# Kernel tuning notes

Measured on AMD Instinct MI355X. Metric: run time of the kernel, lower is better.

The kernel has to match this reference:

```python
import jax, jax.numpy as jnp
import numpy as np

N = 128   # n_features == out_dim (required by the Christoffel permutes)
H = 256   # MLP hidden width of forward_func
B = 16    # batch size (state_batch is [2B, N])
EPS_G = 1e-4
EPS_DG = 1e-6
EPS_V = 1e-6


def setup_inputs() -> dict:
    key = jax.random.key(0)
    ks = jax.random.split(key, 6)
    return {
        "t": jax.random.uniform(ks[0], (), dtype=jnp.float32),
        "state_batch": jax.random.normal(ks[1], (2 * B, N), dtype=jnp.float32) * 0.1,
        "x0_batch": jax.random.normal(ks[2], (B, N), dtype=jnp.float32),
        "x1_batch": jax.random.normal(ks[3], (B, N), dtype=jnp.float32),
        "W1": jax.random.normal(ks[4], (N, H), dtype=jnp.float32) / np.float32(np.sqrt(N)),
        "b1": jnp.zeros((H,), dtype=jnp.float32),
        "W2": jax.random.normal(ks[5], (H, N), dtype=jnp.float32) / np.float32(np.sqrt(H)),
        "b2": jnp.zeros((N,), dtype=jnp.float32),
    }


def reference(t, state_batch, x0_batch, x1_batch, W1, b1, W2, b2):
    def f(x):  # forward_func, per-sample: [N] -> [N]
        return jnp.tanh(x @ W1 + b1) @ W2 + b2

    def metric(x):  # G(x) = J J^T + 1e-4 I, per-sample: [N] -> [N, N]
        J = jax.jacrev(f)(x)                      # [N, N], matches per-output grad loop
        return J @ J.T + EPS_G * jnp.eye(N, dtype=x.dtype)

    deviation, dev_velocity = jnp.split(state_batch, 2, axis=0)  # each [B, N]
    window = 4.0 * t * (1.0 - t)
    # x along the perturbed straight path
    x = x0_batch + t * (x1_batch - x0_batch) + window * deviation  # [B, N]

    # dG[b, i, j, k] = dG_ij/dx_k -- replaces the out_dim^2 autograd.grad loop
    dG = jax.vmap(jax.jacfwd(metric))(x)  # [B, N, N, N]
    nrm = jnp.sqrt(jnp.sum(dG * dG, axis=(1, 2, 3), keepdims=True))
    dG = dG / (nrm + EPS_DG)

    # Christoffel-like symbols
    Gamma = 0.5 * (dG + jnp.transpose(dG, (0, 2, 1, 3)) - jnp.transpose(dG, (0, 3, 1, 2)))
    a = -jnp.einsum('bijk,bj,bk->bi', Gamma, dev_velocity, dev_velocity)
    a = a / (jnp.linalg.norm(dev_velocity, axis=1, keepdims=True) + EPS_V)

    restoration = -0.1 * deviation
    return jnp.concatenate([dev_velocity, a + restoration], axis=0)  # [2B, N]
```

## Files before the change

### kernel.cpp

```cpp
#include <hip/hip_runtime.h>
#include <math.h>


static constexpr int OFF_W2T  = 0;
static constexpr int OFF_S    = 32768;
static constexpr int OFF_Q    = 98304;
static constexpr int OFF_D    = 163840;
static constexpr int OFF_C    = 167936;
static constexpr int OFF_UV   = 172032;
static constexpr int OFF_AV   = 176128;
static constexpr int OFF_VN   = 180224;
static constexpr int OFF_SUM  = 180240;
static constexpr int OFF_PT   = 180256;
static constexpr int OFF_PN   = OFF_PT + 16 * 32768;

__global__ __launch_bounds__(256) void k_stage1(const float* __restrict__ tptr,
                                                const float* __restrict__ state,
                                                const float* __restrict__ x0,
                                                const float* __restrict__ x1,
                                                const float* __restrict__ W1,
                                                const float* __restrict__ b1,
                                                const float* __restrict__ W2,
                                                float* __restrict__ ws,
                                                float* __restrict__ out) {
    __shared__ __align__(16) float smem[2 * 32 * 34];
    int blk = blockIdx.x;
    int tid = threadIdx.x;

    if (blk < 64) {
        float* Ai = smem;
        float* Aj = smem + 1088;
        int m0 = (blk >> 3) * 32, n0 = (blk & 7) * 32;
        int lx = tid & 31, lr = tid >> 5;
        int tx = tid & 15, ty = tid >> 4;
        float a00 = 0, a01 = 0, a10 = 0, a11 = 0;
        for (int kc = 0; kc < 128; kc += 32) {
            #pragma unroll
            for (int i = 0; i < 4; ++i) {
                int k = lr + 8 * i;
                Ai[k * 34 + lx] = W1[(kc + k) * 256 + m0 + lx];
                Aj[k * 34 + lx] = W1[(kc + k) * 256 + n0 + lx];
            }
            __syncthreads();
            #pragma unroll
            for (int k = 0; k < 32; ++k) {
                float2 a = *(const float2*)&Ai[k * 34 + 2 * ty];
                float2 b = *(const float2*)&Aj[k * 34 + 2 * tx];
                a00 += a.x * b.x; a01 += a.x * b.y;
                a10 += a.y * b.x; a11 += a.y * b.y;
            }
            __syncthreads();
        }
        float* S = ws + OFF_S;
        int m = m0 + 2 * ty, n = n0 + 2 * tx;
        S[m * 256 + n]           = a00;
        S[m * 256 + n + 1]       = a01;
        S[(m + 1) * 256 + n]     = a10;
        S[(m + 1) * 256 + n + 1] = a11;
    } else if (blk < 128) {
        float* Xi = smem;
        float* Xj = smem + 1088;
        int bq = blk - 64;
        int m0 = (bq >> 3) * 32, n0 = (bq & 7) * 32;
        int lx = tid & 31, lr = tid >> 5;
        int tx = tid & 15, ty = tid >> 4;
        float a00 = 0, a01 = 0, a10 = 0, a11 = 0;
        for (int kc = 0; kc < 128; kc += 32) {
            #pragma unroll
            for (int i = 0; i < 4; ++i) {
                Xi[lx * 34 + lr + 8 * i] = W2[(m0 + lr + 8 * i) * 128 + kc + lx];
                Xj[lx * 34 + lr + 8 * i] = W2[(n0 + lr + 8 * i) * 128 + kc + lx];
            }
            __syncthreads();
            #pragma unroll
            for (int k = 0; k < 32; ++k) {
                float2 a = *(const float2*)&Xi[k * 34 + 2 * ty];
                float2 b = *(const float2*)&Xj[k * 34 + 2 * tx];
                a00 += a.x * b.x; a01 += a.x * b.y;
                a10 += a.y * b.x; a11 += a.y * b.y;
            }
            __syncthreads();
        }
        float* Q = ws + OFF_Q;
        int m = m0 + 2 * ty, n = n0 + 2 * tx;
        Q[m * 256 + n]           = a00;
        Q[m * 256 + n + 1]       = a01;
        Q[(m + 1) * 256 + n]     = a10;
        Q[(m + 1) * 256 + n + 1] = a11;
    } else if (blk < 160) {
        float* tile = smem;
        int b2 = blk - 128;
        int c0 = (b2 & 3) * 32, r0 = (b2 >> 2) * 32;
        int tx = tid & 31, ty = tid >> 5;
        #pragma unroll
        for (int i = 0; i < 32; i += 8)
            tile[(ty + i) * 33 + tx] = W2[(r0 + ty + i) * 128 + c0 + tx];
        __syncthreads();
        float* W2T = ws + OFF_W2T;
        #pragma unroll
        for (int i = 0; i < 32; i += 8)
            W2T[(c0 + ty + i) * 256 + r0 + tx] = tile[tx * 33 + ty + i];
    } else {
        int b = blk - 160;
        float* xs  = smem;
        float* vs  = smem + 128;
        float* red = smem + 256;
        float t = tptr[0];
        float w = 4.f * t * (1.f - t);
        if (tid == 0) ws[OFF_SUM + b] = 0.f;
        if (tid < 128) {
            float dev = state[b * 128 + tid];
            float v   = state[(16 + b) * 128 + tid];
            float xv  = x0[b * 128 + tid] + t * (x1[b * 128 + tid] - x0[b * 128 + tid]) + w * dev;
            xs[tid] = xv;
            vs[tid] = v;
            out[b * 128 + tid] = v;
            red[tid] = v * v;
        }
        __syncthreads();
        for (int s = 64; s > 0; s >>= 1) {
            if (tid < s) red[tid] += red[tid + s];
            __syncthreads();
        }
        if (tid == 0) ws[OFF_VN + b] = sqrtf(red[0]);

        int m = tid;
        float h = b1[m], uvm = 0.f;
        #pragma unroll 8
        for (int k = 0; k < 128; ++k) {
            float wv = W1[k * 256 + m];
            h   += xs[k] * wv;
            uvm += vs[k] * wv;
        }
        float z  = tanhf(h);
        float dd = 1.f - z * z;
        float cc = -2.f * z * dd;
        const float4* w2r = (const float4*)&W2[m * 128];
        const float4* vs4 = (const float4*)vs;
        float avm = 0.f;
        #pragma unroll 8
        for (int j4 = 0; j4 < 32; ++j4) {
            float4 ww = w2r[j4];
            float4 vv = vs4[j4];
            avm += ww.x * vv.x + ww.y * vv.y + ww.z * vv.z + ww.w * vv.w;
        }
        ws[OFF_D  + b * 256 + m] = dd;
        ws[OFF_C  + b * 256 + m] = cc;
        ws[OFF_UV + b * 256 + m] = uvm;
        ws[OFF_AV + b * 256 + m] = avm;
    }
}

__global__ __launch_bounds__(256) void k_pmat3(const float* __restrict__ Smat,
                                               const float* __restrict__ dall,
                                               const float* __restrict__ W2,
                                               float* __restrict__ PT,
                                               float* __restrict__ Pn) {
    __shared__ __align__(16) float ST[32 * 36];
    __shared__ __align__(16) float YT[32 * 68];
    int b = blockIdx.z, mt = blockIdx.y, jt = blockIdx.x;
    int m0 = mt * 32, j0 = jt * 64;
    const float* dvec = dall + b * 256;
    int tid = threadIdx.x;
    int n = tid >> 3, c4 = (tid & 7) * 4;
    int ty = tid >> 5, tx = tid & 31;
    float acc[4][2] = {};
    for (int nc = 0; nc < 256; nc += 32) {
        *(float4*)&ST[n * 36 + c4] = *(const float4*)&Smat[(nc + n) * 256 + m0 + c4];
        float dn = dvec[nc + n];
        #pragma unroll
        for (int i = 0; i < 2; ++i) {
            int col = c4 + 32 * i;
            float4 wv = *(const float4*)&W2[(nc + n) * 128 + j0 + col];
            wv.x *= dn; wv.y *= dn; wv.z *= dn; wv.w *= dn;
            *(float4*)&YT[n * 68 + col] = wv;
        }
        __syncthreads();
        #pragma unroll 8
        for (int k = 0; k < 32; ++k) {
            float4 a  = *(const float4*)&ST[k * 36 + 4 * ty];
            float2 bb = *(const float2*)&YT[k * 68 + 2 * tx];
            acc[0][0] += a.x * bb.x; acc[0][1] += a.x * bb.y;
            acc[1][0] += a.y * bb.x; acc[1][1] += a.y * bb.y;
            acc[2][0] += a.z * bb.x; acc[2][1] += a.z * bb.y;
            acc[3][0] += a.w * bb.x; acc[3][1] += a.w * bb.y;
        }
        __syncthreads();
    }
    float* ptb = PT + b * 32768;
    float* pnb = Pn + b * 32768;
    #pragma unroll
    for (int jj = 0; jj < 2; ++jj) {
        float4 v = make_float4(acc[0][jj], acc[1][jj], acc[2][jj], acc[3][jj]);
        *(float4*)&ptb[(j0 + 2 * tx + jj) * 256 + m0 + 4 * ty] = v;
    }
    #pragma unroll
    for (int ii = 0; ii < 4; ++ii) {
        float2 v = make_float2(acc[ii][0], acc[ii][1]);
        *(float2*)&pnb[(m0 + 4 * ty + ii) * 128 + j0 + 2 * tx] = v;
    }
}

__global__ __launch_bounds__(256) void k_fnorm5(const float* __restrict__ PT,
                                                const float* __restrict__ W2T,
                                                const float* __restrict__ Smat,
                                                const float* __restrict__ Qmat,
                                                const float* __restrict__ call,
                                                float* __restrict__ sums) {
    __shared__ __align__(16) float lds[16384];
    int b = blockIdx.y;
    int idx = blockIdx.x;
    int tj = 0;
    while ((tj + 1) * (tj + 2) / 2 <= idx) ++tj;
    int ti = idx - tj * (tj + 1) / 2;
    int mi0 = ti * 32, mj0 = tj * 32;
    int tid = threadIdx.x;
    float* PiT = lds;
    float* PjT = lds + 4096;
    float* WiT = lds + 8192;
    float* WjT = lds + 12288;
    const float* ptb = PT + b * 32768;
    int jr = tid >> 3, jc4 = (tid & 7) * 4;
    #pragma unroll
    for (int it = 0; it < 4; ++it) {
        int j = jr + 32 * it;
        *(float4*)&PiT[j * 32 + jc4] = *(const float4*)&ptb[j * 256 + mi0 + jc4];
        *(float4*)&PjT[j * 32 + jc4] = *(const float4*)&ptb[j * 256 + mj0 + jc4];
        *(float4*)&WiT[j * 32 + jc4] = *(const float4*)&W2T[j * 256 + mi0 + jc4];
        *(float4*)&WjT[j * 32 + jc4] = *(const float4*)&W2T[j * 256 + mj0 + jc4];
    }
    __syncthreads();
    int w = tid >> 6, s = tid & 63;
    int ty = s >> 3, tx = s & 7;
    float r[4][4] = {}, f[4][4] = {}, g[4][4] = {};
    int jbase = 32 * w;
    #pragma unroll 4
    for (int jj = 0; jj < 32; ++jj) {
        int j = jbase + jj;
        float4 pi4 = *(const float4*)&PiT[j * 32 + 4 * ty];
        float4 pj4 = *(const float4*)&PjT[j * 32 + 4 * tx];
        float4 wi4 = *(const float4*)&WiT[j * 32 + 4 * ty];
        float4 wj4 = *(const float4*)&WjT[j * 32 + 4 * tx];
        float pi[4] = {pi4.x, pi4.y, pi4.z, pi4.w};
        float pj[4] = {pj4.x, pj4.y, pj4.z, pj4.w};
        float wi[4] = {wi4.x, wi4.y, wi4.z, wi4.w};
        float wj[4] = {wj4.x, wj4.y, wj4.z, wj4.w};
        #pragma unroll
        for (int ii = 0; ii < 4; ++ii)
            #pragma unroll
            for (int kk = 0; kk < 4; ++kk) {
                r[ii][kk] += pi[ii] * pj[kk];
                f[ii][kk] += pi[ii] * wj[kk];
                g[ii][kk] += pj[kk] * wi[ii];
            }
    }
    __syncthreads();
    {
        float* scr = lds;
        int base = tid * 49;
        #pragma unroll
        for (int ii = 0; ii < 4; ++ii)
            #pragma unroll
            for (int kk = 0; kk < 4; ++kk) {
                scr[base + ii * 4 + kk]      = r[ii][kk];
                scr[base + 16 + ii * 4 + kk] = f[ii][kk];
                scr[base + 32 + ii * 4 + kk] = g[ii][kk];
            }
    }
    __syncthreads();
    if (tid < 64) {
        const float* scr = lds;
        float tr[16], tf[16], tg[16];
        #pragma unroll
        for (int k = 0; k < 16; ++k) {
            tr[k] = scr[tid * 49 + k]           + scr[(tid + 64) * 49 + k]
                  + scr[(tid + 128) * 49 + k]   + scr[(tid + 192) * 49 + k];
            tf[k] = scr[tid * 49 + 16 + k]      + scr[(tid + 64) * 49 + 16 + k]
                  + scr[(tid + 128) * 49 + 16 + k] + scr[(tid + 192) * 49 + 16 + k];
            tg[k] = scr[tid * 49 + 32 + k]      + scr[(tid + 64) * 49 + 32 + k]
                  + scr[(tid + 128) * 49 + 32 + k] + scr[(tid + 192) * 49 + 32 + k];
        }
        const float* cb = call + b * 256;
        int mi = mi0 + 4 * (tid >> 3), mj = mj0 + 4 * (tid & 7);
        float4 ce4 = *(const float4*)&cb[mj];
        float ce[4] = {ce4.x, ce4.y, ce4.z, ce4.w};
        float sum = 0.f;
        #pragma unroll
        for (int ii = 0; ii < 4; ++ii) {
            float ci = cb[mi + ii];
            float4 S4 = *(const float4*)&Smat[(mi + ii) * 256 + mj];
            float4 Q4 = *(const float4*)&Qmat[(mi + ii) * 256 + mj];
            float Sv[4] = {S4.x, S4.y, S4.z, S4.w};
            float Qv[4] = {Q4.x, Q4.y, Q4.z, Q4.w};
            #pragma unroll
            for (int kk = 0; kk < 4; ++kk)
                sum += ci * ce[kk] * Sv[kk] * (Qv[kk] * tr[ii * 4 + kk] + tf[ii * 4 + kk] * tg[ii * 4 + kk]);
        }
        if (ti < tj) sum *= 2.f;
        #pragma unroll
        for (int off = 32; off > 0; off >>= 1)
            sum += __shfl_down(sum, off);
        if (tid == 0) atomicAdd(&sums[b], sum);
    }
}

__global__ __launch_bounds__(256) void k_fin3(const float* __restrict__ state,
                                              const float* __restrict__ W2,
                                              float* __restrict__ ws,
                                              float* __restrict__ out) {
    int b = blockIdx.x;
    int tid = threadIdx.x;
    __shared__ float vs[128], g1[256], g2[256], red[256];
    __shared__ float snrm;
    if (tid < 128) vs[tid] = state[(16 + b) * 128 + tid];
    if (tid == 0) {
        float tot = atomicAdd(&ws[OFF_SUM + b], 0.0f);
        snrm = sqrtf(fmaxf(2.f * tot, 0.f));
    }
    __syncthreads();

    const float* ptb = ws + OFF_PT + b * 32768;
    const float* pnb = ws + OFF_PN + b * 32768;
    int m = tid;
    float pv = 0.f;
    #pragma unroll 8
    for (int j = 0; j < 128; ++j)
        pv += ptb[j * 256 + m] * vs[j];
    float cc  = ws[OFF_C  + b * 256 + m];
    float uvm = ws[OFF_UV + b * 256 + m];
    float avm = ws[OFF_AV + b * 256 + m];
    g1[m] = cc * pv  * uvm;
    g2[m] = cc * avm * uvm;
    __syncthreads();

    int i = tid & 127, half = tid >> 7;
    int mmlo = half * 128;
    float raw = 0.f;
    #pragma unroll 8
    for (int mm = mmlo; mm < mmlo + 128; ++mm)
        raw += W2[mm * 128 + i] * g1[mm] + pnb[mm * 128 + i] * g2[mm];
    red[tid] = raw;
    __syncthreads();
    if (tid < 128) {
        float rawt = red[tid] + red[tid + 128];
        float vn = ws[OFF_VN + b];
        float a  = -0.5f * rawt / ((snrm + 1e-6f) * (vn + 1e-6f));
        out[(16 + b) * 128 + tid] = a - 0.1f * state[b * 128 + tid];
    }
}

extern "C" void kernel_launch(void* const* d_in, const int* in_sizes, int n_in,
                              void* d_out, int out_size, void* d_ws, size_t ws_size,
                              hipStream_t stream) {
    (void)in_sizes; (void)n_in; (void)out_size; (void)ws_size;
    const float* t     = (const float*)d_in[0];
    const float* state = (const float*)d_in[1];
    const float* x0    = (const float*)d_in[2];
    const float* x1    = (const float*)d_in[3];
    const float* W1    = (const float*)d_in[4];
    const float* b1    = (const float*)d_in[5];
    const float* W2    = (const float*)d_in[6];
    float* out = (float*)d_out;
    float* ws  = (float*)d_ws;

    k_stage1<<<176, 256, 0, stream>>>(t, state, x0, x1, W1, b1, W2, ws, out);
    k_pmat3<<<dim3(2, 8, 16), 256, 0, stream>>>(ws + OFF_S, ws + OFF_D, W2,
                                                ws + OFF_PT, ws + OFF_PN);
    k_fnorm5<<<dim3(36, 16), 256, 0, stream>>>(ws + OFF_PT, ws + OFF_W2T, ws + OFF_S,
                                               ws + OFF_Q, ws + OFF_C, ws + OFF_SUM);
    k_fin3<<<16, 256, 0, stream>>>(state, W2, ws, out);
}
```

Baseline: 122.5 us.

## Fuse fnorm and final kernels with per-batch atomic counter handoff

New measurement: 115.0 us. -6.1%, faster.

```diff
diff --git a/kernel.cpp b/kernel.cpp
--- a/kernel.cpp
+++ b/kernel.cpp
@@ -11,7 +11,8 @@
 static constexpr int OFF_AV   = 176128;
 static constexpr int OFF_VN   = 180224;
 static constexpr int OFF_SUM  = 180240;
-static constexpr int OFF_PT   = 180256;
+static constexpr int OFF_CNT  = 180256;
+static constexpr int OFF_PT   = 180272;
 static constexpr int OFF_PN   = OFF_PT + 16 * 32768;
 
 __global__ __launch_bounds__(256) void k_stage1(const float* __restrict__ tptr,
@@ -107,7 +108,10 @@
         float* red = smem + 256;
         float t = tptr[0];
         float w = 4.f * t * (1.f - t);
-        if (tid == 0) ws[OFF_SUM + b] = 0.f;
+        if (tid == 0) {
+            ws[OFF_SUM + b] = 0.f;
+            ((int*)(ws + OFF_CNT))[b] = 0;
+        }
         if (tid < 128) {
             float dev = state[b * 128 + tid];
             float v   = state[(16 + b) * 128 + tid];
@@ -201,60 +205,117 @@
     }
 }
 
-__global__ __launch_bounds__(256) void k_fnorm5(const float* __restrict__ PT,
-                                                const float* __restrict__ W2T,
-                                                const float* __restrict__ Smat,
-                                                const float* __restrict__ Qmat,
-                                                const float* __restrict__ call,
-                                                float* __restrict__ sums) {
-    __shared__ __align__(16) float lds[16384];
-    int b = blockIdx.y;
-    int idx = blockIdx.x;
+__global__ __launch_bounds__(256, 3) void k_fnorm6(const float* __restrict__ state,
+                                                   const float* __restrict__ W2,
+                                                   float* __restrict__ ws,
+                                                   float* __restrict__ out) {
+    __shared__ __align__(16) float lds[12544];
+    int blk = blockIdx.x;
+    int tid = threadIdx.x;
+    int* cnt = (int*)(ws + OFF_CNT);
+
+    if (blk < 16) {
+        int b = blk;
+        const float* ptb = ws + OFF_PT + b * 32768;
+        const float* pnb = ws + OFF_PN + b * 32768;
+        float* vs   = lds;
+        float* g1   = lds + 128;
+        float* g2   = lds + 384;
+        float* red  = lds + 640;
+        float* snrm = lds + 900;
+        if (tid < 128) vs[tid] = state[(16 + b) * 128 + tid];
+        __syncthreads();
+
+        int m = tid;
+        float pv = 0.f;
+        #pragma unroll 8
+        for (int j = 0; j < 128; ++j)
+            pv += ptb[j * 256 + m] * vs[j];
+        float cc  = ws[OFF_C  + b * 256 + m];
+        float uvm = ws[OFF_UV + b * 256 + m];
+        float avm = ws[OFF_AV + b * 256 + m];
+        g1[m] = cc * pv  * uvm;
+        g2[m] = cc * avm * uvm;
+        __syncthreads();
+
+        int i = tid & 127, half = tid >> 7;
+        int mmlo = half * 128;
+        float raw = 0.f;
+        #pragma unroll 8
+        for (int mm = mmlo; mm < mmlo + 128; ++mm)
+            raw += W2[mm * 128 + i] * g1[mm] + pnb[mm * 128 + i] * g2[mm];
+        red[tid] = raw;
+        __syncthreads();
+
+        if (tid == 0) {
+            while (atomicAdd(&cnt[b], 0) < 36) __builtin_amdgcn_s_sleep(2);
+            __threadfence();
+            float tot = atomicAdd(&ws[OFF_SUM + b], 0.0f);
+            snrm[0] = sqrtf(fmaxf(2.f * tot, 0.f));
+        }
+        __syncthreads();
+        if (tid < 128) {
+            float rawt = red[tid] + red[tid + 128];
+            float vn = ws[OFF_VN + b];
+            float a  = -0.5f * rawt / ((snrm[0] + 1e-6f) * (vn + 1e-6f));
+            out[(16 + b) * 128 + tid] = a - 0.1f * state[b * 128 + tid];
+        }
+        return;
+    }
+
+    int q   = blk - 16;
+    int idx = q >> 4;
+    int b   = q & 15;
     int tj = 0;
     while ((tj + 1) * (tj + 2) / 2 <= idx) ++tj;
     int ti = idx - tj * (tj + 1) / 2;
     int mi0 = ti * 32, mj0 = tj * 32;
-    int tid = threadIdx.x;
     float* PiT = lds;
-    float* PjT = lds + 4096;
-    float* WiT = lds + 8192;
-    float* WjT = lds + 12288;
-    const float* ptb = PT + b * 32768;
+    float* PjT = lds + 2048;
+    float* WiT = lds + 4096;
+    float* WjT = lds + 6144;
+    const float* ptb = ws + OFF_PT + b * 32768;
+    const float* W2T = ws + OFF_W2T;
+    const float* Smat = ws + OFF_S;
+    const float* Qmat = ws + OFF_Q;
     int jr = tid >> 3, jc4 = (tid & 7) * 4;
-    #pragma unroll
-    for (int it = 0; it < 4; ++it) {
-        int j = jr + 32 * it;
-        *(float4*)&PiT[j * 32 + jc4] = *(const float4*)&ptb[j * 256 + mi0 + jc4];
-        *(float4*)&PjT[j * 32 + jc4] = *(const float4*)&ptb[j * 256 + mj0 + jc4];
-        *(float4*)&WiT[j * 32 + jc4] = *(const float4*)&W2T[j * 256 + mi0 + jc4];
-        *(float4*)&WjT[j * 32 + jc4] = *(const float4*)&W2T[j * 256 + mj0 + jc4];
-    }
-    __syncthreads();
     int w = tid >> 6, s = tid & 63;
     int ty = s >> 3, tx = s & 7;
     float r[4][4] = {}, f[4][4] = {}, g[4][4] = {};
-    int jbase = 32 * w;
-    #pragma unroll 4
-    for (int jj = 0; jj < 32; ++jj) {
-        int j = jbase + jj;
-        float4 pi4 = *(const float4*)&PiT[j * 32 + 4 * ty];
-        float4 pj4 = *(const float4*)&PjT[j * 32 + 4 * tx];
-        float4 wi4 = *(const float4*)&WiT[j * 32 + 4 * ty];
-        float4 wj4 = *(const float4*)&WjT[j * 32 + 4 * tx];
-        float pi[4] = {pi4.x, pi4.y, pi4.z, pi4.w};
-        float pj[4] = {pj4.x, pj4.y, pj4.z, pj4.w};
-        float wi[4] = {wi4.x, wi4.y, wi4.z, wi4.w};
-        float wj[4] = {wj4.x, wj4.y, wj4.z, wj4.w};
-        #pragma unroll
-        for (int ii = 0; ii < 4; ++ii)
-            #pragma unroll
-            for (int kk = 0; kk < 4; ++kk) {
-                r[ii][kk] += pi[ii] * pj[kk];
-                f[ii][kk] += pi[ii] * wj[kk];
-                g[ii][kk] += pj[kk] * wi[ii];
-            }
-    }
-    __syncthreads();
+    #pragma unroll
+    for (int rr = 0; rr < 2; ++rr) {
+        #pragma unroll
+        for (int it = 0; it < 2; ++it) {
+            int l = jr + 32 * it;
+            int j = 32 * (l >> 4) + 16 * rr + (l & 15);
+            *(float4*)&PiT[l * 32 + jc4] = *(const float4*)&ptb[j * 256 + mi0 + jc4];
+            *(float4*)&PjT[l * 32 + jc4] = *(const float4*)&ptb[j * 256 + mj0 + jc4];
+            *(float4*)&WiT[l * 32 + jc4] = *(const float4*)&W2T[j * 256 + mi0 + jc4];
+            *(float4*)&WjT[l * 32 + jc4] = *(const float4*)&W2T[j * 256 + mj0 + jc4];
+        }
+        __syncthreads();
+        #pragma unroll 4
+        for (int jj = 0; jj < 16; ++jj) {
+            int l = 16 * w + jj;
+            float4 pi4 = *(const float4*)&PiT[l * 32 + 4 * ty];
+            float4 pj4 = *(const float4*)&PjT[l * 32 + 4 * tx];
+            float4 wi4 = *(const float4*)&WiT[l * 32 + 4 * ty];
+            float4 wj4 = *(const float4*)&WjT[l * 32 + 4 * tx];
+            float pi[4] = {pi4.x, pi4.y, pi4.z, pi4.w};
+            float pj[4] = {pj4.x, pj4.y, pj4.z, pj4.w};
+            float wi[4] = {wi4.x, wi4.y, wi4.z, wi4.w};
+            float wj[4] = {wj4.x, wj4.y, wj4.z, wj4.w};
+            #pragma unroll
+            for (int ii = 0; ii < 4; ++ii)
+                #pragma unroll
+                for (int kk = 0; kk < 4; ++kk) {
+                    r[ii][kk] += pi[ii] * pj[kk];
+                    f[ii][kk] += pi[ii] * wj[kk];
+                    g[ii][kk] += pj[kk] * wi[ii];
+                }
+        }
+        __syncthreads();
+    }
     {
         float* scr = lds;
         int base = tid * 49;
@@ -280,7 +341,7 @@
             tg[k] = scr[tid * 49 + 32 + k]      + scr[(tid + 64) * 49 + 32 + k]
                   + scr[(tid + 128) * 49 + 32 + k] + scr[(tid + 192) * 49 + 32 + k];
         }
-        const float* cb = call + b * 256;
+        const float* cb = ws + OFF_C + b * 256;
         int mi = mi0 + 4 * (tid >> 3), mj = mj0 + 4 * (tid & 7);
         float4 ce4 = *(const float4*)&cb[mj];
         float ce[4] = {ce4.x, ce4.y, ce4.z, ce4.w};
@@ -300,52 +361,11 @@
         #pragma unroll
         for (int off = 32; off > 0; off >>= 1)
             sum += __shfl_down(sum, off);
-        if (tid == 0) atomicAdd(&sums[b], sum);
-    }
-}
-
-__global__ __launch_bounds__(256) void k_fin3(const float* __restrict__ state,
-                                              const float* __restrict__ W2,
-                                              float* __restrict__ ws,
-                                              float* __restrict__ out) {
-    int b = blockIdx.x;
-    int tid = threadIdx.x;
-    __shared__ float vs[128], g1[256], g2[256], red[256];
-    __shared__ float snrm;
-    if (tid < 128) vs[tid] = state[(16 + b) * 128 + tid];
-    if (tid == 0) {
-        float tot = atomicAdd(&ws[OFF_SUM + b], 0.0f);
-        snrm = sqrtf(fmaxf(2.f * tot, 0.f));
-    }
-    __syncthreads();
-
-    const float* ptb = ws + OFF_PT + b * 32768;
-    const float* pnb = ws + OFF_PN + b * 32768;
-    int m = tid;
-    float pv = 0.f;
-    #pragma unroll 8
-    for (int j = 0; j < 128; ++j)
-        pv += ptb[j * 256 + m] * vs[j];
-    float cc  = ws[OFF_C  + b * 256 + m];
-    float uvm = ws[OFF_UV + b * 256 + m];
-    float avm = ws[OFF_AV + b * 256 + m];
-    g1[m] = cc * pv  * uvm;
-    g2[m] = cc * avm * uvm;
-    __syncthreads();
-
-    int i = tid & 127, half = tid >> 7;
-    int mmlo = half * 128;
-    float raw = 0.f;
-    #pragma unroll 8
-    for (int mm = mmlo; mm < mmlo + 128; ++mm)
-        raw += W2[mm * 128 + i] * g1[mm] + pnb[mm * 128 + i] * g2[mm];
-    red[tid] = raw;
-    __syncthreads();
-    if (tid < 128) {
-        float rawt = red[tid] + red[tid + 128];
-        float vn = ws[OFF_VN + b];
-        float a  = -0.5f * rawt / ((snrm + 1e-6f) * (vn + 1e-6f));
-        out[(16 + b) * 128 + tid] = a - 0.1f * state[b * 128 + tid];
+        if (tid == 0) {
+            atomicAdd(&ws[OFF_SUM + b], sum);
+            __threadfence();
+            atomicAdd(&cnt[b], 1);
+        }
     }
 }
 
@@ -366,7 +386,5 @@
     k_stage1<<<176, 256, 0, stream>>>(t, state, x0, x1, W1, b1, W2, ws, out);
     k_pmat3<<<dim3(2, 8, 16), 256, 0, stream>>>(ws + OFF_S, ws + OFF_D, W2,
                                                 ws + OFF_PT, ws + OFF_PN);
-    k_fnorm5<<<dim3(36, 16), 256, 0, stream>>>(ws + OFF_PT, ws + OFF_W2T, ws + OFF_S,
-                                               ws + OFF_Q, ws + OFF_C, ws + OFF_SUM);
-    k_fin3<<<16, 256, 0, stream>>>(state, W2, ws, out);
+    k_fnorm6<<<592, 256, 0, stream>>>(state, W2, ws, out);
 }
```
